# Optimization experiments

Hardware: AMD Instinct MI355X
Metric: run time of the kernel (lower is better)

Reference implementation:

```python
import jax, jax.numpy as jnp
import numpy as np

SOFTMAX_TEMP = 0.01  # config['networks']['matcher_block']['softmax_temp']
B, WINDOW, C, N, WIDTH = 2, 2, 64, 400, 256


def setup_inputs() -> dict:
    key = jax.random.key(0)
    k1, k2, k3 = jax.random.split(key, 3)
    BW = B * WINDOW
    keypoint_scores = jax.random.uniform(k1, (BW, 1, N), dtype=jnp.float32)
    keypoint_desc = jax.random.normal(k2, (BW, C, N), dtype=jnp.float32)
    desc_dense = jax.random.normal(k3, (BW, C, WIDTH, WIDTH), dtype=jnp.float32)
    # pairing indices exactly as built in SoftmaxRefMatcher.__init__
    tgt_ids, src_ids = [], []
    for b in range(B):
        for w in range(WINDOW - 1):
            for t in range(w + 1, WINDOW):
                src_ids.append(w + b * WINDOW)
                tgt_ids.append(t + b * WINDOW)
    return {
        "keypoint_scores": keypoint_scores,
        "keypoint_desc": keypoint_desc,
        "desc_dense": desc_dense,
        "tgt_ids": jnp.array(tgt_ids, dtype=jnp.int32),
        "src_ids": jnp.array(src_ids, dtype=jnp.int32),
    }


def _l2_normalize(x):
    # F.normalize(x, dim=1), eps=1e-12
    return x / jnp.maximum(jnp.linalg.norm(x, axis=1, keepdims=True), 1e-12)


def reference(keypoint_scores, keypoint_desc, desc_dense, tgt_ids, src_ids):
    BW, Cdim, H, W = desc_dense.shape
    HW = H * W
    # src_coords_dense: meshgrid('ij') -> coords[k] = (u=k%W, v=k//W)
    hw = jnp.arange(HW)
    coords = jnp.stack([(hw % W).astype(jnp.float32),
                        (hw // W).astype(jnp.float32)], axis=1)  # [HW, 2]

    src_desc = _l2_normalize(desc_dense.reshape(BW, Cdim, HW))[src_ids]  # [P, C, HW]
    tgt_desc = _l2_normalize(keypoint_desc)[tgt_ids]                     # [P, C, N]

    match_vals = jnp.einsum('pcn,pcm->pnm', tgt_desc, src_desc)          # [P, N, HW]
    soft_match = jax.nn.softmax(match_vals / SOFTMAX_TEMP, axis=2)
    pseudo_coords = jnp.einsum('pnm,mk->pnk', soft_match, coords)        # [P, N, 2]

    tgt_scores = keypoint_scores[tgt_ids]
    return pseudo_coords, tgt_scores, tgt_ids, src_ids
```

## Files before the change

kernel.cpp:

```cpp
#include <hip/hip_runtime.h>
#include <math.h>

#define NPAIR  2
#define KDIM   64
#define NKP    400
#define NTILE  28
#define HWPIX  65536
#define MREF   70.0f
#define LOG2E  1.44269504f

#define BFRAG_DW (NPAIR*NTILE*2*2*256)

using frag_ab = __attribute__((ext_vector_type(8))) short;
using f32x4   = __attribute__((ext_vector_type(4))) float;

__device__ __forceinline__ unsigned short f2bf(float f){
    unsigned u = __builtin_bit_cast(unsigned, f);
    u += 0x7fffu + ((u >> 16) & 1u);
    return (unsigned short)(u >> 16);
}
__device__ __forceinline__ float bf2f(unsigned short h){
    unsigned u = ((unsigned)h) << 16;
    return __builtin_bit_cast(float, u);
}

__global__ __launch_bounds__(256) void prep_kernel(
    const float* __restrict__ ksc, const float* __restrict__ kd,
    const int* __restrict__ tgt_ids, const int* __restrict__ src_ids,
    unsigned* __restrict__ wsu, float* __restrict__ out)
{
    __shared__ float xs[KDIM][33];
    __shared__ float inv_s[32];
    int d = blockIdx.x, p = blockIdx.y, t = threadIdx.x;
    int tgt = tgt_ids[p];
    int nl = t & 31, c0 = t >> 5;
    #pragma unroll
    for (int cc = 0; cc < 8; ++cc){
        int c = cc*8 + c0;
        int n = d*32 + nl;
        xs[c][nl] = (n < NKP) ? kd[(tgt*KDIM + c)*NKP + n] : 0.f;
    }
    __syncthreads();
    if (t < 32){
        float s = 0.f;
        #pragma unroll
        for (int c = 0; c < KDIM; ++c){ float v = xs[c][t]; s = fmaf(v, v, s); }
        inv_s[t] = 1.f / fmaxf(sqrtf(s), 1e-12f);
    }
    __syncthreads();
    {
        int l = t & 63, rk = t >> 6;
        int rt = rk >> 1, ks = rk & 1;
        int cl = l & 15, g = l >> 4;
        int nloc = rt*16 + cl;
        float inv = inv_s[nloc];
        int k0 = ks*32 + g*8;
        unsigned hu[4], lu[4];
        #pragma unroll
        for (int j2 = 0; j2 < 4; ++j2){
            float xa = xs[k0 + 2*j2    ][nloc] * inv;
            float xb = xs[k0 + 2*j2 + 1][nloc] * inv;
            unsigned short ha = f2bf(xa), hb = f2bf(xb);
            unsigned short la = f2bf(xa - bf2f(ha)), lb = f2bf(xb - bf2f(hb));
            hu[j2] = (unsigned)ha | ((unsigned)hb << 16);
            lu[j2] = (unsigned)la | ((unsigned)lb << 16);
        }
        int nt = d*2 + rt;
        unsigned base = (unsigned)(((p*NTILE + nt)*2 + ks)*2)*256 + l*4;
        *(uint4*)&wsu[base]       = make_uint4(hu[0], hu[1], hu[2], hu[3]);
        *(uint4*)&wsu[base + 256] = make_uint4(lu[0], lu[1], lu[2], lu[3]);
    }
    if (t < 32){
        int n = d*32 + t;
        if (n < NKP) out[NPAIR*NKP*2 + p*NKP + n] = ksc[tgt*NKP + n];
    }
    if (d == 0 && t == 0){
        out[NPAIR*NKP*3 + p]         = (float)tgt;
        out[NPAIR*NKP*3 + NPAIR + p] = (float)src_ids[p];
    }
}

__global__ __launch_bounds__(256, 4) void match_kernel(
    const float* __restrict__ dd, const int* __restrict__ src_ids,
    const unsigned* __restrict__ wsu, float* __restrict__ part)
{
    __shared__ unsigned lds[8192];
    __shared__ float ssp[256];
    __shared__ float invn_s[128];
    int mb = blockIdx.x, p = blockIdx.y, t = threadIdx.x;
    int w = t >> 6, l = t & 63;
    int g = l >> 4;

    const unsigned* wB = wsu + (unsigned)p*28672 + (unsigned)l*4;
    uint4 Bb0[4], Bb1[4];
    #pragma unroll
    for (int k = 0; k < 4; ++k) Bb0[k] = *(const uint4*)(wB + k*256);
    #pragma unroll
    for (int k = 0; k < 4; ++k) Bb1[k] = *(const uint4*)(wB + 1024 + k*256);

    const float* plane = dd + (size_t)src_ids[p]*KDIM*HWPIX + mb*128;

    {
        int m = t & 127, kh = t >> 7;
        unsigned sw = (unsigned)(m & 7);
        float ssum = 0.f;
        const float* cp = plane + m + (size_t)kh*32*HWPIX;
        #pragma unroll
        for (int s2l = 0; s2l < 4; ++s2l){
            float v[8];
            #pragma unroll
            for (int j = 0; j < 8; ++j) v[j] = cp[(size_t)(s2l*8 + j)*HWPIX];
            unsigned hq[4], lq[4];
            #pragma unroll
            for (int q = 0; q < 4; ++q){
                float a = v[2*q], b = v[2*q+1];
                ssum = fmaf(a, a, ssum);
                ssum = fmaf(b, b, ssum);
                unsigned ta = (__builtin_bit_cast(unsigned, a) + 0x8000u) & 0xFFFF0000u;
                unsigned tb = (__builtin_bit_cast(unsigned, b) + 0x8000u) & 0xFFFF0000u;
                float la = a - __builtin_bit_cast(float, ta);
                float lb = b - __builtin_bit_cast(float, tb);
                hq[q] = __builtin_amdgcn_perm(tb, ta, 0x07060302u);
                lq[q] = __builtin_amdgcn_perm(__builtin_bit_cast(unsigned, lb),
                                              __builtin_bit_cast(unsigned, la), 0x07060302u);
            }
            unsigned slot = ((unsigned)(kh*4 + s2l)) ^ sw;
            unsigned dwb = (unsigned)m*32 + slot*4;
            *(uint4*)&lds[dwb]        = make_uint4(hq[0], hq[1], hq[2], hq[3]);
            *(uint4*)&lds[4096 + dwb] = make_uint4(lq[0], lq[1], lq[2], lq[3]);
        }
        ssp[t] = ssum;
    }
    __syncthreads();
    if (t < 128)
        invn_s[t] = (100.f * LOG2E) / fmaxf(sqrtf(ssp[t] + ssp[t + 128]), 1e-12f);
    __syncthreads();

    int mloc0 = w*32;
    uint4 Ac[2][4];
    #pragma unroll
    for (int mt = 0; mt < 2; ++mt){
        unsigned m = (unsigned)(mloc0 + mt*16 + (l & 15));
        unsigned sw = m & 7;
        #pragma unroll
        for (int k = 0; k < 4; ++k){
            unsigned slot = (((unsigned)(k >> 1))*4 + (unsigned)g) ^ sw;
            Ac[mt][k] = *(const uint4*)&lds[(unsigned)(k & 1)*4096 + m*32 + slot*4];
        }
    }
    __syncthreads();

    const float mref2 = MREF * LOG2E;
    float invm8[2][4], ub_[2];
    #pragma unroll
    for (int mt = 0; mt < 2; ++mt){
        ub_[mt] = (float)(mloc0 + mt*16 + g*4);
        #pragma unroll
        for (int r = 0; r < 4; ++r)
            invm8[mt][r] = invn_s[mloc0 + mt*16 + g*4 + r];
    }

    f32x4 acc0[2], acc1[2];
    float* wp = (float*)lds;

    auto zacc = [&](f32x4* a){
        a[0] = (f32x4){0.f,0.f,0.f,0.f};
        a[1] = (f32x4){0.f,0.f,0.f,0.f};
    };
    auto unit = [&](const uint4* Bq, f32x4* a2){
        #pragma unroll
        for (int ks = 0; ks < 2; ++ks){
            frag_ab bH  = __builtin_bit_cast(frag_ab, Bq[ks*2]);
            frag_ab bL  = __builtin_bit_cast(frag_ab, Bq[ks*2 + 1]);
            frag_ab a0H = __builtin_bit_cast(frag_ab, Ac[0][ks*2]);
            frag_ab a0L = __builtin_bit_cast(frag_ab, Ac[0][ks*2 + 1]);
            frag_ab a1H = __builtin_bit_cast(frag_ab, Ac[1][ks*2]);
            frag_ab a1L = __builtin_bit_cast(frag_ab, Ac[1][ks*2 + 1]);
            a2[0] = __builtin_amdgcn_mfma_f32_16x16x32_bf16(a0H, bH, a2[0], 0, 0, 0);
            a2[1] = __builtin_amdgcn_mfma_f32_16x16x32_bf16(a1H, bH, a2[1], 0, 0, 0);
            a2[0] = __builtin_amdgcn_mfma_f32_16x16x32_bf16(a0H, bL, a2[0], 0, 0, 0);
            a2[1] = __builtin_amdgcn_mfma_f32_16x16x32_bf16(a1H, bL, a2[1], 0, 0, 0);
            a2[0] = __builtin_amdgcn_mfma_f32_16x16x32_bf16(a0L, bH, a2[0], 0, 0, 0);
            a2[1] = __builtin_amdgcn_mfma_f32_16x16x32_bf16(a1L, bH, a2[1], 0, 0, 0);
        }
    };
    auto loadB = [&](int nt, uint4* B){
        const unsigned* q = wB + (unsigned)nt*1024;
        #pragma unroll
        for (int k = 0; k < 4; ++k) B[k] = *(const uint4*)(q + k*256);
    };
    auto epi = [&](const f32x4* a2, int nt){
        float Ssum = 0.f, Usum = 0.f;
        #pragma unroll
        for (int mt = 0; mt < 2; ++mt){
            float e0 = __builtin_amdgcn_exp2f(fmaf(a2[mt][0], invm8[mt][0], -mref2));
            float e1 = __builtin_amdgcn_exp2f(fmaf(a2[mt][1], invm8[mt][1], -mref2));
            float e2 = __builtin_amdgcn_exp2f(fmaf(a2[mt][2], invm8[mt][2], -mref2));
            float e3 = __builtin_amdgcn_exp2f(fmaf(a2[mt][3], invm8[mt][3], -mref2));
            float Sm = (e0 + e1) + (e2 + e3);
            float Um = fmaf(e2, 2.f, e1);
            Um = fmaf(e3, 3.f, Um);
            Um = fmaf(ub_[mt], Sm, Um);
            Ssum += Sm; Usum += Um;
        }
        Ssum += __shfl_xor(Ssum, 16); Usum += __shfl_xor(Usum, 16);
        Ssum += __shfl_xor(Ssum, 32); Usum += __shfl_xor(Usum, 32);
        if (l < 16)
            *(float2*)&wp[((unsigned)(w*NTILE + nt)*16 + (unsigned)l)*2] =
                make_float2(Ssum, Usum);
    };

    zacc(acc0); unit(Bb0, acc0);
    #pragma unroll 1
    for (int j = 0; j < 13; ++j){
        loadB(2*j + 2, Bb0);
        zacc(acc1); unit(Bb1, acc1);
        epi(acc0, 2*j);
        loadB(2*j + 3, Bb1);
        zacc(acc0); unit(Bb0, acc0);
        epi(acc1, 2*j + 1);
    }
    zacc(acc1); unit(Bb1, acc1);
    epi(acc0, 26);
    epi(acc1, 27);

    __syncthreads();
    for (int idx = t; idx < NTILE*16; idx += 256){
        int nt = idx >> 4, cl = idx & 15;
        float S = 0.f, U = 0.f;
        #pragma unroll
        for (int ww = 0; ww < 4; ++ww){
            float2 q = *(const float2*)&wp[((unsigned)(ww*NTILE + nt)*16 + (unsigned)cl)*2];
            S += q.x; U += q.y;
        }
        *(float2*)&part[(((size_t)p*NTILE + nt)*512 + mb)*32 + cl*2] =
            make_float2(S, U);
    }
}

__global__ __launch_bounds__(256) void merge_kernel(
    const float* __restrict__ part, float* __restrict__ out)
{
    __shared__ float red[3][4][16];
    int nt = blockIdx.x, p = blockIdx.y, t = threadIdx.x;
    int j = t & 15, mb0 = t >> 4;
    const float* base = part + ((size_t)(p*NTILE + nt)*512)*32;
    float S = 0.f, U = 0.f, V = 0.f;
    #pragma unroll 4
    for (int k = 0; k < 32; ++k){
        int mbk = mb0 + k*16;
        float2 q = *(const float2*)&base[(mbk*16 + j)*2];
        S += q.x;
        U += q.y + (float)((mbk & 1)*128)*q.x;
        V = fmaf((float)(mbk >> 1), q.x, V);
    }
    S += __shfl_xor(S, 16); U += __shfl_xor(U, 16); V += __shfl_xor(V, 16);
    S += __shfl_xor(S, 32); U += __shfl_xor(U, 32); V += __shfl_xor(V, 32);
    int w = t >> 6, l = t & 63;
    if (l < 16){ red[0][w][j] = S; red[1][w][j] = U; red[2][w][j] = V; }
    __syncthreads();
    if (t < 16){
        float Sf = red[0][0][t] + red[0][1][t] + red[0][2][t] + red[0][3][t];
        float Uf = red[1][0][t] + red[1][1][t] + red[1][2][t] + red[1][3][t];
        float Vf = red[2][0][t] + red[2][1][t] + red[2][2][t] + red[2][3][t];
        int n = nt*16 + t;
        out[(p*NKP + n)*2 + 0] = Uf / Sf;
        out[(p*NKP + n)*2 + 1] = Vf / Sf;
    }
}

extern "C" void kernel_launch(void* const* d_in, const int* in_sizes, int n_in,
                              void* d_out, int out_size, void* d_ws, size_t ws_size,
                              hipStream_t stream)
{
    const float* ksc     = (const float*)d_in[0];
    const float* kd      = (const float*)d_in[1];
    const float* dd      = (const float*)d_in[2];
    const int*   tgt_ids = (const int*)d_in[3];
    const int*   src_ids = (const int*)d_in[4];
    float* out = (float*)d_out;
    unsigned* wsu = (unsigned*)d_ws;
    float* part = (float*)d_ws + BFRAG_DW;

    prep_kernel <<<dim3(14, NPAIR),  256, 0, stream>>>(ksc, kd, tgt_ids, src_ids, wsu, out);
    match_kernel<<<dim3(512, NPAIR), 256, 0, stream>>>(dd, src_ids, wsu, part);
    merge_kernel<<<dim3(25, NPAIR),  256, 0, stream>>>(part, out);
}
```

Before: 126.6 us.

## Stage B fragments in shared LDS via async loads, load A directly into registers

Each block now fetches the per-tile B fragments once, using async global-to-LDS loads into a 4-slot ring shared by all four waves. Previously every wave loaded its own copy of B into registers. The A operand is read from global memory straight into MFMA register layout, which drops the LDS staging pass and two barriers, and per-pixel norms are reduced with wave shuffles. In exchange, each iteration now ends with a block barrier, and the global reads for A are less contiguous, in 16-float runs.

```diff
diff --git a/kernel.cpp b/kernel.cpp
--- a/kernel.cpp
+++ b/kernel.cpp
@@ -22,6 +22,11 @@
 __device__ __forceinline__ float bf2f(unsigned short h){
     unsigned u = ((unsigned)h) << 16;
     return __builtin_bit_cast(float, u);
+}
+__device__ __forceinline__ void async16(unsigned* lds, const unsigned* g){
+    __builtin_amdgcn_global_load_lds(
+        (const __attribute__((address_space(1))) unsigned*)g,
+        (__attribute__((address_space(3))) unsigned*)lds, 16, 0, 0);
 }
 
 __global__ __launch_bounds__(256) void prep_kernel(
@@ -84,38 +89,39 @@
     const float* __restrict__ dd, const int* __restrict__ src_ids,
     const unsigned* __restrict__ wsu, float* __restrict__ part)
 {
-    __shared__ unsigned lds[8192];
-    __shared__ float ssp[256];
+    __shared__ unsigned Bst[4][1024];
     __shared__ float invn_s[128];
+    __shared__ float wp[4*NTILE*16*2];
     int mb = blockIdx.x, p = blockIdx.y, t = threadIdx.x;
     int w = t >> 6, l = t & 63;
-    int g = l >> 4;
-
-    const unsigned* wB = wsu + (unsigned)p*28672 + (unsigned)l*4;
-    uint4 Bb0[4], Bb1[4];
+    int cl = l & 15, g = l >> 4;
+    int mloc0 = w*32;
+
+    const unsigned* wBp = wsu + (unsigned)p*(NTILE*1024) + (unsigned)t*4;
+    auto bload = [&](int nt){
+        async16(&Bst[nt & 3][(unsigned)w*256], wBp + (unsigned)nt*1024);
+    };
+
+    bload(0); bload(1);
+
+    const float* ap = dd + (size_t)src_ids[p]*KDIM*HWPIX + (size_t)mb*128
+                    + (unsigned)(mloc0 + cl);
+    uint4 Ac[2][4];
     #pragma unroll
-    for (int k = 0; k < 4; ++k) Bb0[k] = *(const uint4*)(wB + k*256);
-    #pragma unroll
-    for (int k = 0; k < 4; ++k) Bb1[k] = *(const uint4*)(wB + 1024 + k*256);
-
-    const float* plane = dd + (size_t)src_ids[p]*KDIM*HWPIX + mb*128;
-
-    {
-        int m = t & 127, kh = t >> 7;
-        unsigned sw = (unsigned)(m & 7);
-        float ssum = 0.f;
-        const float* cp = plane + m + (size_t)kh*32*HWPIX;
-        #pragma unroll
-        for (int s2l = 0; s2l < 4; ++s2l){
+    for (int mt = 0; mt < 2; ++mt){
+        float ss = 0.f;
+        #pragma unroll
+        for (int ks = 0; ks < 2; ++ks){
             float v[8];
             #pragma unroll
-            for (int j = 0; j < 8; ++j) v[j] = cp[(size_t)(s2l*8 + j)*HWPIX];
+            for (int j = 0; j < 8; ++j)
+                v[j] = ap[(size_t)(ks*32 + g*8 + j)*HWPIX + mt*16];
             unsigned hq[4], lq[4];
             #pragma unroll
             for (int q = 0; q < 4; ++q){
                 float a = v[2*q], b = v[2*q+1];
-                ssum = fmaf(a, a, ssum);
-                ssum = fmaf(b, b, ssum);
+                ss = fmaf(a, a, ss);
+                ss = fmaf(b, b, ss);
                 unsigned ta = (__builtin_bit_cast(unsigned, a) + 0x8000u) & 0xFFFF0000u;
                 unsigned tb = (__builtin_bit_cast(unsigned, b) + 0x8000u) & 0xFFFF0000u;
                 float la = a - __builtin_bit_cast(float, ta);
@@ -124,54 +130,37 @@
                 lq[q] = __builtin_amdgcn_perm(__builtin_bit_cast(unsigned, lb),
                                               __builtin_bit_cast(unsigned, la), 0x07060302u);
             }
-            unsigned slot = ((unsigned)(kh*4 + s2l)) ^ sw;
-            unsigned dwb = (unsigned)m*32 + slot*4;
-            *(uint4*)&lds[dwb]        = make_uint4(hq[0], hq[1], hq[2], hq[3]);
-            *(uint4*)&lds[4096 + dwb] = make_uint4(lq[0], lq[1], lq[2], lq[3]);
-        }
-        ssp[t] = ssum;
-    }
-    __syncthreads();
-    if (t < 128)
-        invn_s[t] = (100.f * LOG2E) / fmaxf(sqrtf(ssp[t] + ssp[t + 128]), 1e-12f);
-    __syncthreads();
-
-    int mloc0 = w*32;
-    uint4 Ac[2][4];
+            Ac[mt][ks*2 + 0] = make_uint4(hq[0], hq[1], hq[2], hq[3]);
+            Ac[mt][ks*2 + 1] = make_uint4(lq[0], lq[1], lq[2], lq[3]);
+        }
+        ss += __shfl_xor(ss, 16);
+        ss += __shfl_xor(ss, 32);
+        if (g == 0)
+            invn_s[mloc0 + mt*16 + cl] = (100.f*LOG2E) / fmaxf(sqrtf(ss), 1e-12f);
+    }
+    __syncthreads();
+
+    const float mref2 = MREF * LOG2E;
+    float invm8[2][4], ub2[2];
     #pragma unroll
     for (int mt = 0; mt < 2; ++mt){
-        unsigned m = (unsigned)(mloc0 + mt*16 + (l & 15));
-        unsigned sw = m & 7;
-        #pragma unroll
-        for (int k = 0; k < 4; ++k){
-            unsigned slot = (((unsigned)(k >> 1))*4 + (unsigned)g) ^ sw;
-            Ac[mt][k] = *(const uint4*)&lds[(unsigned)(k & 1)*4096 + m*32 + slot*4];
-        }
-    }
-    __syncthreads();
-
-    const float mref2 = MREF * LOG2E;
-    float invm8[2][4], ub_[2];
-    #pragma unroll
-    for (int mt = 0; mt < 2; ++mt){
-        ub_[mt] = (float)(mloc0 + mt*16 + g*4);
+        ub2[mt] = (float)(mloc0 + mt*16 + g*4);
         #pragma unroll
         for (int r = 0; r < 4; ++r)
             invm8[mt][r] = invn_s[mloc0 + mt*16 + g*4 + r];
     }
 
     f32x4 acc0[2], acc1[2];
-    float* wp = (float*)lds;
-
     auto zacc = [&](f32x4* a){
         a[0] = (f32x4){0.f,0.f,0.f,0.f};
         a[1] = (f32x4){0.f,0.f,0.f,0.f};
     };
-    auto unit = [&](const uint4* Bq, f32x4* a2){
+    auto unit = [&](int nt, f32x4* a2){
+        const unsigned* Bb = &Bst[nt & 3][0];
         #pragma unroll
         for (int ks = 0; ks < 2; ++ks){
-            frag_ab bH  = __builtin_bit_cast(frag_ab, Bq[ks*2]);
-            frag_ab bL  = __builtin_bit_cast(frag_ab, Bq[ks*2 + 1]);
+            frag_ab bH  = __builtin_bit_cast(frag_ab, *(const uint4*)&Bb[(ks*2+0)*256 + l*4]);
+            frag_ab bL  = __builtin_bit_cast(frag_ab, *(const uint4*)&Bb[(ks*2+1)*256 + l*4]);
             frag_ab a0H = __builtin_bit_cast(frag_ab, Ac[0][ks*2]);
             frag_ab a0L = __builtin_bit_cast(frag_ab, Ac[0][ks*2 + 1]);
             frag_ab a1H = __builtin_bit_cast(frag_ab, Ac[1][ks*2]);
@@ -184,11 +173,6 @@
             a2[1] = __builtin_amdgcn_mfma_f32_16x16x32_bf16(a1L, bH, a2[1], 0, 0, 0);
         }
     };
-    auto loadB = [&](int nt, uint4* B){
-        const unsigned* q = wB + (unsigned)nt*1024;
-        #pragma unroll
-        for (int k = 0; k < 4; ++k) B[k] = *(const uint4*)(q + k*256);
-    };
     auto epi = [&](const f32x4* a2, int nt){
         float Ssum = 0.f, Usum = 0.f;
         #pragma unroll
@@ -200,7 +184,7 @@
             float Sm = (e0 + e1) + (e2 + e3);
             float Um = fmaf(e2, 2.f, e1);
             Um = fmaf(e3, 3.f, Um);
-            Um = fmaf(ub_[mt], Sm, Um);
+            Um = fmaf(ub2[mt], Sm, Um);
             Ssum += Sm; Usum += Um;
         }
         Ssum += __shfl_xor(Ssum, 16); Usum += __shfl_xor(Usum, 16);
@@ -210,30 +194,25 @@
                 make_float2(Ssum, Usum);
     };
 
-    zacc(acc0); unit(Bb0, acc0);
     #pragma unroll 1
-    for (int j = 0; j < 13; ++j){
-        loadB(2*j + 2, Bb0);
-        zacc(acc1); unit(Bb1, acc1);
+    for (int j = 0; j < 14; ++j){
+        if (j < 13){ bload(2*j + 2); bload(2*j + 3); }
+        zacc(acc0); unit(2*j,     acc0);
+        zacc(acc1); unit(2*j + 1, acc1);
         epi(acc0, 2*j);
-        loadB(2*j + 3, Bb1);
-        zacc(acc0); unit(Bb0, acc0);
         epi(acc1, 2*j + 1);
-    }
-    zacc(acc1); unit(Bb1, acc1);
-    epi(acc0, 26);
-    epi(acc1, 27);
-
-    __syncthreads();
+        __syncthreads();
+    }
+
     for (int idx = t; idx < NTILE*16; idx += 256){
-        int nt = idx >> 4, cl = idx & 15;
+        int nt = idx >> 4, cc = idx & 15;
         float S = 0.f, U = 0.f;
         #pragma unroll
         for (int ww = 0; ww < 4; ++ww){
-            float2 q = *(const float2*)&wp[((unsigned)(ww*NTILE + nt)*16 + (unsigned)cl)*2];
+            float2 q = *(const float2*)&wp[((unsigned)(ww*NTILE + nt)*16 + (unsigned)cc)*2];
             S += q.x; U += q.y;
         }
-        *(float2*)&part[(((size_t)p*NTILE + nt)*512 + mb)*32 + cl*2] =
+        *(float2*)&part[(((size_t)p*NTILE + nt)*512 + mb)*32 + cc*2] =
             make_float2(S, U);
     }
 }
```

Result: slower. 129.6 us (+2.4%).
